# Kernel tuning notes

Hardware: AMD Instinct MI355X
Metric: run time of the kernel (lower is better)

Reference implementation:

```python
import jax, jax.numpy as jnp
import numpy as np

H = 8          # heads
D = 512        # d_model
DK = D // H    # per-head dim
FF = 2048      # feed-forward size
STACKS = 3
VOCAB = 5000
PAD = 0
LN_EPS = 1e-6


def _layer_norm(x, g, b):
    mu = jnp.mean(x, axis=-1, keepdims=True)
    var = jnp.mean(jnp.square(x - mu), axis=-1, keepdims=True)
    return (x - mu) * jax.lax.rsqrt(var + LN_EPS) * g + b


def _positional_encoding(T, d):
    pos = jnp.arange(T, dtype=jnp.float32)[:, None]                      # (T,1)
    div = jnp.exp(jnp.arange(0, d, 2, dtype=jnp.float32) * (-np.log(10000.0) / d))
    pe = jnp.zeros((T, d), dtype=jnp.float32)
    pe = pe.at[:, 0::2].set(jnp.sin(pos * div))
    pe = pe.at[:, 1::2].set(jnp.cos(pos * div))
    return pe  # (T, D)


def _mha(q_in, kv, wq, bq, wk, bk, wv, bv, wo, bo, mask):
    B, Tq, _ = q_in.shape
    Tk = kv.shape[1]
    q = (q_in @ wq + bq).reshape(B, Tq, H, DK).transpose(0, 2, 1, 3)   # (B,H,Tq,DK)
    k = (kv @ wk + bk).reshape(B, Tk, H, DK).transpose(0, 2, 1, 3)
    v = (kv @ wv + bv).reshape(B, Tk, H, DK).transpose(0, 2, 1, 3)
    score = jnp.einsum('bhqd,bhkd->bhqk', q, k) / jnp.sqrt(jnp.float32(DK))
    if mask is not None:
        score = jnp.where(mask, score, jnp.float32(-1e9))
    p = jax.nn.softmax(score, axis=-1)
    out = jnp.einsum('bhqk,bhkd->bhqd', p, v)
    out = out.transpose(0, 2, 1, 3).reshape(B, Tq, D)
    return out @ wo + bo


def setup_inputs() -> dict:
    key = jax.random.key(0)
    ks = jax.random.split(key, 24)
    s = 0.02
    inp = {
        'target': jax.random.randint(ks[0], (32, 256), 0, VOCAB),
        'memory': jax.random.normal(ks[1], (32, 1024, D), dtype=jnp.float32),
        'emb': jax.random.normal(ks[2], (VOCAB, D), dtype=jnp.float32) * s,
        'ln_g': jnp.ones((D,), jnp.float32),
        'ln_b': jnp.zeros((D,), jnp.float32),
        'ff_w1': jax.random.normal(ks[3], (D, FF), jnp.float32) * s,
        'ff_b1': jnp.zeros((FF,), jnp.float32),
        'ff_w2': jax.random.normal(ks[4], (FF, D), jnp.float32) * s,
        'ff_b2': jnp.zeros((D,), jnp.float32),
    }
    names = ['wq', 'wk', 'wv', 'wo']
    for i, n in enumerate(names):
        inp['sa_' + n] = jax.random.normal(ks[5 + i], (D, D), jnp.float32) * s
        inp['sa_b' + n[1]] = jnp.zeros((D,), jnp.float32)
        inp['ca_' + n] = jax.random.normal(ks[9 + i], (D, D), jnp.float32) * s
        inp['ca_b' + n[1]] = jnp.zeros((D,), jnp.float32)
    return inp


def reference(target, memory, emb, ln_g, ln_b, ff_w1, ff_b1, ff_w2, ff_b2,
              sa_wq, sa_bq, sa_wk, sa_bk, sa_wv, sa_bv, sa_wo, sa_bo,
              ca_wq, ca_bq, ca_wk, ca_bk, ca_wv, ca_bv, ca_wo, ca_bo):
    B, T = target.shape
    x = emb[target] * jnp.sqrt(jnp.float32(D))              # (B,T,D)
    x = x + _positional_encoding(T, D)                       # dropout = identity (eval)
    # masks: causal & pad for self-attn; cross-attn mask is all-ones -> skip
    pad = (target != PAD)[:, None, :, None]                  # (B,1,T,1)
    causal = jnp.tril(jnp.ones((T, T), dtype=bool))          # (T,T)
    tgt_mask = pad & causal                                  # (B,1,T,T)
    out = x
    for _ in range(STACKS):  # shared parameters
        n = _layer_norm(out, ln_g, ln_b)
        out = out + _mha(n, n, sa_wq, sa_bq, sa_wk, sa_bk, sa_wv, sa_bv, sa_wo, sa_bo, tgt_mask)
        n = _layer_norm(out, ln_g, ln_b)
        out = out + _mha(n, memory, ca_wq, ca_bq, ca_wk, ca_bk, ca_wv, ca_bv, ca_wo, ca_bo, None)
        n = _layer_norm(out, ln_g, ln_b)
        out = out + (jax.nn.relu(n @ ff_w1 + ff_b1) @ ff_w2 + ff_b2)
    return _layer_norm(out, ln_g, ln_b)
```

## Files before the change

kernel.cpp:

```cpp
#include <hip/hip_runtime.h>
#include <cstdint>
#include <cstddef>

typedef unsigned short u16;
typedef __bf16 bf16x8 __attribute__((ext_vector_type(8)));
typedef float f32x4 __attribute__((ext_vector_type(4)));

#define DEV static __device__ __forceinline__

#define QSCALE 0.18033688011112042f

DEV u16 f2bf(float f) { unsigned v; __builtin_memcpy(&v, &f, 4); v += 0x7fffu + ((v >> 16) & 1u); return (u16)(v >> 16); }

DEV void gll16(const void* g, void* l) {
    __builtin_amdgcn_global_load_lds(
        (__attribute__((address_space(1))) void*)g,
        (__attribute__((address_space(3))) void*)l, 16, 0, 0);
}

__global__ void embed_pe(const int* __restrict__ tgt, const float* __restrict__ emb,
                         float* __restrict__ x)
{
    const int bt = blockIdx.x;
    const int t  = bt & 255;
    const int tok = tgt[bt];
    for (int d = threadIdx.x; d < 512; d += 256) {
        float e  = emb[(size_t)tok * 512 + d] * 22.62741699796952f;
        int   d0 = d & ~1;
        float ang = (float)t * expf((float)d0 * (-9.210340371976184f / 512.f));
        float pe  = (d & 1) ? cosf(ang) : sinf(ang);
        x[(size_t)bt * 512 + d] = e + pe;
    }
}

__global__ void transpose_k(const float* __restrict__ in, u16* __restrict__ out,
                            int K, int N)
{
    int id = blockIdx.x * 256 + threadIdx.x;
    int k = id / N, n = id % N;
    out[(size_t)n * K + k] = f2bf(in[id]);
}

__global__ void memcast(const float* __restrict__ in, u16* __restrict__ out)
{
    int i = (blockIdx.x * 256 + threadIdx.x) * 4;
    float4 v = *(const float4*)(in + i);
    uint2 w;
    w.x = (unsigned)f2bf(v.x) | ((unsigned)f2bf(v.y) << 16);
    w.y = (unsigned)f2bf(v.z) | ((unsigned)f2bf(v.w) << 16);
    *(uint2*)(out + i) = w;
}

__global__ void concat_bias(const float* __restrict__ a, const float* __restrict__ b,
                            float* __restrict__ out)
{
    int i = blockIdx.x * 256 + threadIdx.x;
    if (i < 512) { out[i] = a[i]; out[512 + i] = b[i]; }
}

template<bool OUTF32>
__global__ void layernorm_k(const float* __restrict__ x, const float* __restrict__ g,
                            const float* __restrict__ b, void* __restrict__ outv)
{
    const int row  = blockIdx.x * 4 + (threadIdx.x >> 6);
    const int lane = threadIdx.x & 63;
    const float* xr = x + (size_t)row * 512;
    float4 v0 = *(const float4*)(xr + lane * 4);
    float4 v1 = *(const float4*)(xr + 256 + lane * 4);
    float s = v0.x + v0.y + v0.z + v0.w + v1.x + v1.y + v1.z + v1.w;
    float q = v0.x*v0.x + v0.y*v0.y + v0.z*v0.z + v0.w*v0.w
            + v1.x*v1.x + v1.y*v1.y + v1.z*v1.z + v1.w*v1.w;
#pragma unroll
    for (int o = 1; o < 64; o <<= 1) { s += __shfl_xor(s, o, 64); q += __shfl_xor(q, o, 64); }
    float mu  = s * (1.f / 512.f);
    float var = q * (1.f / 512.f) - mu * mu;
    float rs  = rsqrtf(fmaxf(var, 0.f) + 1e-6f);

#pragma unroll
    for (int h = 0; h < 2; h++) {
        const int d0 = h * 256 + lane * 4;
        float4 v = h ? v1 : v0;
        float4 gg = *(const float4*)(g + d0);
        float4 bb = *(const float4*)(b + d0);
        float o0 = (v.x - mu) * rs * gg.x + bb.x;
        float o1 = (v.y - mu) * rs * gg.y + bb.y;
        float o2 = (v.z - mu) * rs * gg.z + bb.z;
        float o3 = (v.w - mu) * rs * gg.w + bb.w;
        if (OUTF32) {
            *(float4*)((float*)outv + (size_t)row * 512 + d0) = make_float4(o0, o1, o2, o3);
        } else {
            uint2 w;
            w.x = (unsigned)f2bf(o0) | ((unsigned)f2bf(o1) << 16);
            w.y = (unsigned)f2bf(o2) | ((unsigned)f2bf(o3) << 16);
            *(uint2*)((u16*)outv + (size_t)row * 512 + d0) = w;
        }
    }
}

template<bool OUTF32>
__global__ void ln_sum_k(const float* __restrict__ x, const float* __restrict__ p,
                         const float* __restrict__ g, const float* __restrict__ b,
                         float* __restrict__ xout, void* __restrict__ outv)
{
    const int row  = blockIdx.x * 4 + (threadIdx.x >> 6);
    const int lane = threadIdx.x & 63;
    const size_t base = (size_t)row * 512;
    const float* xr = x + base;
    const float* pa = p + base;
    const float* pb = p + 4194304 + base;
    float4 v0, v1;
    {
        float4 a = *(const float4*)(xr + lane * 4);
        float4 c = *(const float4*)(pa + lane * 4);
        float4 d = *(const float4*)(pb + lane * 4);
        v0 = make_float4(a.x + c.x + d.x, a.y + c.y + d.y, a.z + c.z + d.z, a.w + c.w + d.w);
        a = *(const float4*)(xr + 256 + lane * 4);
        c = *(const float4*)(pa + 256 + lane * 4);
        d = *(const float4*)(pb + 256 + lane * 4);
        v1 = make_float4(a.x + c.x + d.x, a.y + c.y + d.y, a.z + c.z + d.z, a.w + c.w + d.w);
    }
    float s = v0.x + v0.y + v0.z + v0.w + v1.x + v1.y + v1.z + v1.w;
    float q = v0.x*v0.x + v0.y*v0.y + v0.z*v0.z + v0.w*v0.w
            + v1.x*v1.x + v1.y*v1.y + v1.z*v1.z + v1.w*v1.w;
#pragma unroll
    for (int o = 1; o < 64; o <<= 1) { s += __shfl_xor(s, o, 64); q += __shfl_xor(q, o, 64); }
    float mu  = s * (1.f / 512.f);
    float var = q * (1.f / 512.f) - mu * mu;
    float rs  = rsqrtf(fmaxf(var, 0.f) + 1e-6f);

#pragma unroll
    for (int h = 0; h < 2; h++) {
        const int d0 = h * 256 + lane * 4;
        float4 v = h ? v1 : v0;
        if (!OUTF32) *(float4*)(xout + base + d0) = v;
        float4 gg = *(const float4*)(g + d0);
        float4 bb = *(const float4*)(b + d0);
        float o0 = (v.x - mu) * rs * gg.x + bb.x;
        float o1 = (v.y - mu) * rs * gg.y + bb.y;
        float o2 = (v.z - mu) * rs * gg.z + bb.z;
        float o3 = (v.w - mu) * rs * gg.w + bb.w;
        if (OUTF32) {
            *(float4*)((float*)outv + base + d0) = make_float4(o0, o1, o2, o3);
        } else {
            uint2 w;
            w.x = (unsigned)f2bf(o0) | ((unsigned)f2bf(o1) << 16);
            w.y = (unsigned)f2bf(o2) | ((unsigned)f2bf(o3) << 16);
            *(uint2*)((u16*)outv + base + d0) = w;
        }
    }
}

template<int EPI, bool BROW, int BN, int QS, int SPLIT>
__launch_bounds__(256, BN == 64 ? 4 : 2)
__global__ void gemm_bt(const u16* __restrict__ A, int lda,
                        const u16* __restrict__ Bt,
                        const float* __restrict__ bias,
                        void* __restrict__ outp, int ldo, int K)
{
    constexpr int NJ = BN / 32;
    __shared__ u16 As[128 * 32];
    __shared__ u16 Bs[BN * 32];

    const int gx = gridDim.x, gy = gridDim.y;
    const int nwg = gx * gy * gridDim.z;
    int lin = blockIdx.x + gx * (blockIdx.y + gy * blockIdx.z);
    lin = (lin & 7) * (nwg >> 3) + (lin >> 3);
    const int bx = lin % gx;
    const int rem = lin / gx;
    const int by = rem % gy;
    const int bz = rem / gy;

    const int tid  = threadIdx.x;
    const int lane = tid & 63;
    const int wave = tid >> 6;
    const int quad = lane >> 4, l16 = lane & 15;
    const int l4 = lane >> 2, c8 = (lane & 3) * 8;
    const int m0 = by * 128, n0 = bx * BN;
    const int wm = (wave >> 1) * 64, wn = (wave & 1) * (BN / 2);

    const int kc = K / SPLIT;
    const int kbeg = bz * kc;

    f32x4 acc[4][NJ];
#pragma unroll
    for (int i = 0; i < 4; i++)
#pragma unroll
        for (int j = 0; j < NJ; j++) acc[i][j] = f32x4{0.f, 0.f, 0.f, 0.f};

    for (int k0 = kbeg; k0 < kbeg + kc; k0 += 32) {
        __syncthreads();
        gll16(&A[(size_t)(m0 + wave * 32 + l4)      * lda + k0 + c8], &As[(wave * 32) * 32]);
        gll16(&A[(size_t)(m0 + wave * 32 + 16 + l4) * lda + k0 + c8], &As[(wave * 32 + 16) * 32]);
        if (BN == 128) {
            gll16(&Bt[(size_t)(n0 + wave * 32 + l4)      * K + k0 + c8], &Bs[(wave * 32) * 32]);
            gll16(&Bt[(size_t)(n0 + wave * 32 + 16 + l4) * K + k0 + c8], &Bs[(wave * 32 + 16) * 32]);
        } else {
            gll16(&Bt[(size_t)(n0 + wave * 16 + l4) * K + k0 + c8], &Bs[(wave * 16) * 32]);
        }
        __syncthreads();
        bf16x8 af[4], bfr[NJ];
#pragma unroll
        for (int i = 0; i < 4; i++) af[i]  = *(const bf16x8*)&As[(wm + i * 16 + l16) * 32 + quad * 8];
#pragma unroll
        for (int j = 0; j < NJ; j++) bfr[j] = *(const bf16x8*)&Bs[(wn + j * 16 + l16) * 32 + quad * 8];
#pragma unroll
        for (int i = 0; i < 4; i++)
#pragma unroll
            for (int j = 0; j < NJ; j++)
                acc[i][j] = __builtin_amdgcn_mfma_f32_16x16x32_bf16(af[i], bfr[j], acc[i][j], 0, 0, 0);
    }

    const bool dobias = (SPLIT == 1) || (bz == 0);
#pragma unroll
    for (int i = 0; i < 4; i++)
#pragma unroll
        for (int j = 0; j < NJ; j++) {
            const int col = n0 + wn + j * 16 + l16;
            const float bc = BROW ? 0.f : (dobias ? bias[col] : 0.f);
#pragma unroll
            for (int r = 0; r < 4; r++) {
                const int row = m0 + wm + i * 16 + quad * 4 + r;
                const float bv = BROW ? (dobias ? bias[row] : 0.f) : bc;
                float v = acc[i][j][r] + bv;
                if (QS == 1) v *= QSCALE;
                if (QS == 2 && col < 512) v *= QSCALE;
                if (EPI == 1) v = fmaxf(v, 0.f);
                if (EPI == 3) {
                    ((float*)outp)[(size_t)bz * 8192 * ldo + (size_t)row * ldo + col] = v;
                } else {
                    ((u16*)outp)[(size_t)row * ldo + col] = f2bf(v);
                }
            }
        }
}

template<bool SELF>
__launch_bounds__(256, 4)
__global__ void attn(const u16* __restrict__ Qb, int qs,
                     const u16* __restrict__ Kb, int ks, int koff,
                     const u16* __restrict__ Vt, int ldv,
                     const int* __restrict__ target,
                     u16* __restrict__ Ob, int Tk)
{
    __shared__ u16 KsL[64 * 32], KsH[64 * 32];
    __shared__ u16 VsL[64 * 32], VsH[64 * 32];
    __shared__ float P32[4][16][68];
    __shared__ int needtail;
    const int tid  = threadIdx.x;
    const int lane = tid & 63;
    const int wave = tid >> 6;
    const int quad = lane >> 4, l16 = lane & 15;
    const int l4 = lane >> 2, c8 = (lane & 3) * 8;
    const int b = blockIdx.x, h = blockIdx.y, qz = blockIdx.z;
    const int qbase = qz * 64 + wave * 16;
    const int hq = h * 64;

    if (tid == 0) needtail = 0;

    const u16* qr = Qb + (size_t)(b * 256 + qbase + l16) * qs + hq;
    bf16x8 qf0 = *(const bf16x8*)(qr + quad * 8);
    bf16x8 qf1 = *(const bf16x8*)(qr + 32 + quad * 8);

    f32x4 o[4];
#pragma unroll
    for (int t = 0; t < 4; t++) o[t] = f32x4{0.f, 0.f, 0.f, 0.f};
    float ps = 0.f;
    bool rv[4];
    bool inv = false;
    if (SELF) {
#pragma unroll
        for (int r = 0; r < 4; r++) {
            rv[r] = (target[b * 256 + qbase + quad * 4 + r] != 0);
            inv |= !rv[r];
        }
    }
    const bool winv = SELF ? __any(inv) : false;
    __syncthreads();
    if (winv && lane == 0) needtail = 1;
    __syncthreads();
    const int nch = SELF ? (needtail ? (Tk >> 6) : (qz + 1)) : (Tk >> 6);

    const u16* kbase = Kb + (size_t)b * Tk * ks + koff + hq;
    const u16* vbase = Vt + (size_t)hq * ldv + (size_t)b * Tk;
    float* pw = &P32[wave][0][0];

    for (int c = 0; c < nch; c++) {
        const int k0 = c * 64;
        __syncthreads();
        gll16(kbase + (size_t)(k0 + wave * 16 + l4) * ks + c8,      &KsL[(wave * 16) * 32]);
        gll16(kbase + (size_t)(k0 + wave * 16 + l4) * ks + 32 + c8, &KsH[(wave * 16) * 32]);
        gll16(vbase + (size_t)(wave * 16 + l4) * ldv + k0 + c8,      &VsL[(wave * 16) * 32]);
        gll16(vbase + (size_t)(wave * 16 + l4) * ldv + k0 + 32 + c8, &VsH[(wave * 16) * 32]);
        __syncthreads();

        float s[4][4];
#pragma unroll
        for (int g = 0; g < 4; g++) {
            bf16x8 kf0 = *(const bf16x8*)&KsL[(g * 16 + l16) * 32 + quad * 8];
            bf16x8 kf1 = *(const bf16x8*)&KsH[(g * 16 + l16) * 32 + quad * 8];
            f32x4 sv = f32x4{0.f, 0.f, 0.f, 0.f};
            sv = __builtin_amdgcn_mfma_f32_16x16x32_bf16(qf0, kf0, sv, 0, 0, 0);
            sv = __builtin_amdgcn_mfma_f32_16x16x32_bf16(qf1, kf1, sv, 0, 0, 0);
#pragma unroll
            for (int r = 0; r < 4; r++) s[g][r] = sv[r];
        }
        if (SELF) {
            if (k0 + 64 > qbase) {
#pragma unroll
                for (int g = 0; g < 4; g++)
#pragma unroll
                    for (int r = 0; r < 4; r++)
                        if (k0 + g * 16 + l16 > qbase + quad * 4 + r) s[g][r] = -1e9f;
            }
            if (winv) {
#pragma unroll
                for (int g = 0; g < 4; g++)
#pragma unroll
                    for (int r = 0; r < 4; r++)
                        if (!rv[r]) s[g][r] = 0.f;
            }
        }
#pragma unroll
        for (int g = 0; g < 4; g++)
#pragma unroll
            for (int r = 0; r < 4; r++)
                pw[(quad * 4 + r) * 68 + g * 16 + l16] = s[g][r];
        f32x4 ra0 = *(const f32x4*)&pw[l16 * 68 + quad * 8];
        f32x4 ra1 = *(const f32x4*)&pw[l16 * 68 + quad * 8 + 4];
        f32x4 rb0 = *(const f32x4*)&pw[l16 * 68 + 32 + quad * 8];
        f32x4 rb1 = *(const f32x4*)&pw[l16 * 68 + 36 + quad * 8];
        bf16x8 pa0, pa1;
#pragma unroll
        for (int j = 0; j < 4; j++) { float p = exp2f(ra0[j]); ps += p; pa0[j]     = (__bf16)p; }
#pragma unroll
        for (int j = 0; j < 4; j++) { float p = exp2f(ra1[j]); ps += p; pa0[4 + j] = (__bf16)p; }
#pragma unroll
        for (int j = 0; j < 4; j++) { float p = exp2f(rb0[j]); ps += p; pa1[j]     = (__bf16)p; }
#pragma unroll
        for (int j = 0; j < 4; j++) { float p = exp2f(rb1[j]); ps += p; pa1[4 + j] = (__bf16)p; }
#pragma unroll
        for (int t = 0; t < 4; t++) {
            bf16x8 vf0 = *(const bf16x8*)&VsL[(t * 16 + l16) * 32 + quad * 8];
            bf16x8 vf1 = *(const bf16x8*)&VsH[(t * 16 + l16) * 32 + quad * 8];
            o[t] = __builtin_amdgcn_mfma_f32_16x16x32_bf16(pa0, vf0, o[t], 0, 0, 0);
            o[t] = __builtin_amdgcn_mfma_f32_16x16x32_bf16(pa1, vf1, o[t], 0, 0, 0);
        }
    }

    ps += __shfl_xor(ps, 16, 64);
    ps += __shfl_xor(ps, 32, 64);
#pragma unroll
    for (int r = 0; r < 4; r++) {
        const float inv_l = 1.f / __shfl(ps, quad * 4 + r, 64);
        const int tq = qbase + quad * 4 + r;
        u16* orow = Ob + (size_t)(b * 256 + tq) * 512 + hq;
#pragma unroll
        for (int t = 0; t < 4; t++) orow[t * 16 + l16] = f2bf(o[t][r] * inv_l);
    }
}

#define O_X      ((size_t)0)
#define O_N      ((size_t)16777216)
#define O_QK     ((size_t)25165824)
#define O_VTS    ((size_t)41943040)
#define O_ATT    ((size_t)50331648)
#define O_FFN    ((size_t)58720256)
#define O_KVC    ((size_t)92274688)
#define O_VTC    ((size_t)125829120)
#define O_WQKT   ((size_t)159383552)
#define O_SAVT   ((size_t)160432128)
#define O_WOT    ((size_t)160956416)
#define O_CAQT   ((size_t)161480704)
#define O_CAKT   ((size_t)162004992)
#define O_CAVT   ((size_t)162529280)
#define O_CAWOT  ((size_t)163053568)
#define O_FF1T   ((size_t)163577856)
#define O_FF2T   ((size_t)165675008)
#define O_BQK    ((size_t)167772160)

extern "C" void kernel_launch(void* const* d_in, const int* in_sizes, int n_in,
                              void* d_out, int out_size, void* d_ws, size_t ws_size,
                              hipStream_t stream)
{
    const int*   target = (const int*)d_in[0];
    const float* memory = (const float*)d_in[1];
    const float* emb    = (const float*)d_in[2];
    const float* ln_g   = (const float*)d_in[3];
    const float* ln_b   = (const float*)d_in[4];
    const float* ff_w1  = (const float*)d_in[5];
    const float* ff_b1  = (const float*)d_in[6];
    const float* ff_w2  = (const float*)d_in[7];
    const float* ff_b2  = (const float*)d_in[8];
    const float* sa_wq  = (const float*)d_in[9];
    const float* sa_bq  = (const float*)d_in[10];
    const float* ca_wq  = (const float*)d_in[11];
    const float* ca_bq  = (const float*)d_in[12];
    const float* sa_wk  = (const float*)d_in[13];
    const float* sa_bk  = (const float*)d_in[14];
    const float* ca_wk  = (const float*)d_in[15];
    const float* ca_bk  = (const float*)d_in[16];
    const float* sa_wv  = (const float*)d_in[17];
    const float* sa_bv  = (const float*)d_in[18];
    const float* ca_wv  = (const float*)d_in[19];
    const float* ca_bv  = (const float*)d_in[20];
    const float* sa_wo  = (const float*)d_in[21];
    const float* sa_bo  = (const float*)d_in[22];
    const float* ca_wo  = (const float*)d_in[23];
    const float* ca_bo  = (const float*)d_in[24];

    char* ws = (char*)d_ws;
    float* xf   = (float*)(ws + O_X);
    u16* nbuf   = (u16*)(ws + O_N);
    u16* qk     = (u16*)(ws + O_QK);
    u16* qbuf   = (u16*)(ws + O_QK);
    float* ffp  = (float*)(ws + O_QK);
    u16* vts    = (u16*)(ws + O_VTS);
    u16* att    = (u16*)(ws + O_ATT);
    u16* ffn    = (u16*)(ws + O_FFN);
    u16* membf  = (u16*)(ws + O_FFN);
    float* wop  = (float*)(ws + O_FFN);
    u16* kvc    = (u16*)(ws + O_KVC);
    u16* vtc    = (u16*)(ws + O_VTC);
    u16* wqkt   = (u16*)(ws + O_WQKT);
    u16* savt   = (u16*)(ws + O_SAVT);
    u16* wot    = (u16*)(ws + O_WOT);
    u16* caqt   = (u16*)(ws + O_CAQT);
    u16* cakt   = (u16*)(ws + O_CAKT);
    u16* cavt   = (u16*)(ws + O_CAVT);
    u16* cawot  = (u16*)(ws + O_CAWOT);
    u16* ff1t   = (u16*)(ws + O_FF1T);
    u16* ff2t   = (u16*)(ws + O_FF2T);
    float* bqk  = (float*)(ws + O_BQK);

    transpose_k<<<1024, 256, 0, stream>>>(sa_wq, wqkt,             512, 512);
    transpose_k<<<1024, 256, 0, stream>>>(sa_wk, wqkt + 512 * 512, 512, 512);
    transpose_k<<<1024, 256, 0, stream>>>(sa_wv, savt,  512, 512);
    transpose_k<<<1024, 256, 0, stream>>>(sa_wo, wot,   512, 512);
    transpose_k<<<1024, 256, 0, stream>>>(ca_wq, caqt,  512, 512);
    transpose_k<<<1024, 256, 0, stream>>>(ca_wk, cakt,  512, 512);
    transpose_k<<<1024, 256, 0, stream>>>(ca_wv, cavt,  512, 512);
    transpose_k<<<1024, 256, 0, stream>>>(ca_wo, cawot, 512, 512);
    transpose_k<<<4096, 256, 0, stream>>>(ff_w1, ff1t,  512, 2048);
    transpose_k<<<4096, 256, 0, stream>>>(ff_w2, ff2t, 2048, 512);
    concat_bias<<<2, 256, 0, stream>>>(sa_bq, sa_bk, bqk);

    embed_pe<<<8192, 256, 0, stream>>>(target, emb, xf);

    memcast<<<16384, 256, 0, stream>>>(memory, membf);
    gemm_bt<0, false, 64, 0, 1><<<dim3(8, 256), 256, 0, stream>>>(membf, 512, cakt, ca_bk, kvc, 512, 512);
    gemm_bt<0, true,  64, 0, 1><<<dim3(512, 4), 256, 0, stream>>>(cavt, 512, membf, ca_bv, vtc, 32768, 512);

    for (int s = 0; s < 3; s++) {
        if (s == 0)
            layernorm_k<false><<<2048, 256, 0, stream>>>(xf, ln_g, ln_b, nbuf);
        else
            ln_sum_k<false><<<2048, 256, 0, stream>>>(xf, ffp, ln_g, ln_b, xf, nbuf);
        gemm_bt<0, false, 64, 2, 1><<<dim3(16, 64), 256, 0, stream>>>(nbuf, 512, wqkt, bqk, qk, 1024, 512);
        gemm_bt<0, true,  64, 0, 1><<<dim3(128, 4), 256, 0, stream>>>(savt, 512, nbuf, sa_bv, vts, 8192, 512);
        attn<true><<<dim3(32, 8, 4), 256, 0, stream>>>(qk, 1024, qk, 1024, 512, vts, 8192, target, att, 256);
        gemm_bt<3, false, 64, 0, 2><<<dim3(8, 64, 2), 256, 0, stream>>>(att, 512, wot, sa_bo, wop, 512, 512);
        ln_sum_k<false><<<2048, 256, 0, stream>>>(xf, wop, ln_g, ln_b, xf, nbuf);
        gemm_bt<0, false, 64, 1, 1><<<dim3(8, 64), 256, 0, stream>>>(nbuf, 512, caqt, ca_bq, qbuf, 512, 512);
        attn<false><<<dim3(32, 8, 4), 256, 0, stream>>>(qbuf, 512, kvc, 512, 0, vtc, 32768, nullptr, att, 1024);
        gemm_bt<3, false, 64, 0, 2><<<dim3(8, 64, 2), 256, 0, stream>>>(att, 512, cawot, ca_bo, wop, 512, 512);
        ln_sum_k<false><<<2048, 256, 0, stream>>>(xf, wop, ln_g, ln_b, xf, nbuf);
        gemm_bt<1, false, 64, 0, 1><<<dim3(32, 64), 256, 0, stream>>>(nbuf, 512, ff1t, ff_b1, ffn, 2048, 512);
        gemm_bt<3, false, 64, 0, 2><<<dim3(8, 64, 2), 256, 0, stream>>>(ffn, 2048, ff2t, ff_b2, ffp, 512, 2048);
    }

    ln_sum_k<true><<<2048, 256, 0, stream>>>(xf, ffp, ln_g, ln_b, xf, d_out);
}
```

Baseline: 926.1 us.

## Process two query tiles per attention block with double-buffered K/V loads

The attention kernel now handles two 64-query tiles per block, so each K/V chunk staged in LDS is reused across twice as many query rows. K/V chunks are double-buffered, with the next chunk's async global-to-LDS load issued before computing the current one, leaving one barrier per iteration. Grid z is halved and launch bounds are relaxed to 2 blocks, which lowers parallelism and coarsens causal chunk skipping in exchange for less load traffic and better overlap.

```diff
diff --git a/kernel.cpp b/kernel.cpp
--- a/kernel.cpp
+++ b/kernel.cpp
@@ -234,16 +234,15 @@
         }
 }
 
-template<bool SELF>
-__launch_bounds__(256, 4)
+template<bool SELF, int QT>
+__launch_bounds__(256, 2)
 __global__ void attn(const u16* __restrict__ Qb, int qs,
                      const u16* __restrict__ Kb, int ks, int koff,
                      const u16* __restrict__ Vt, int ldv,
                      const int* __restrict__ target,
                      u16* __restrict__ Ob, int Tk)
 {
-    __shared__ u16 KsL[64 * 32], KsH[64 * 32];
-    __shared__ u16 VsL[64 * 32], VsH[64 * 32];
+    __shared__ u16 KV[2][4][64 * 32];
     __shared__ float P32[4][16][68];
     __shared__ int needtail;
     const int tid  = threadIdx.x;
@@ -252,110 +251,153 @@
     const int quad = lane >> 4, l16 = lane & 15;
     const int l4 = lane >> 2, c8 = (lane & 3) * 8;
     const int b = blockIdx.x, h = blockIdx.y, qz = blockIdx.z;
-    const int qbase = qz * 64 + wave * 16;
     const int hq = h * 64;
 
     if (tid == 0) needtail = 0;
 
-    const u16* qr = Qb + (size_t)(b * 256 + qbase + l16) * qs + hq;
-    bf16x8 qf0 = *(const bf16x8*)(qr + quad * 8);
-    bf16x8 qf1 = *(const bf16x8*)(qr + 32 + quad * 8);
-
-    f32x4 o[4];
-#pragma unroll
-    for (int t = 0; t < 4; t++) o[t] = f32x4{0.f, 0.f, 0.f, 0.f};
-    float ps = 0.f;
-    bool rv[4];
-    bool inv = false;
+    int qbase[QT];
+    bf16x8 qf0[QT], qf1[QT];
+#pragma unroll
+    for (int i = 0; i < QT; i++) {
+        qbase[i] = qz * (64 * QT) + (wave + 4 * i) * 16;
+        const u16* qr = Qb + (size_t)(b * 256 + qbase[i] + l16) * qs + hq;
+        qf0[i] = *(const bf16x8*)(qr + quad * 8);
+        qf1[i] = *(const bf16x8*)(qr + 32 + quad * 8);
+    }
+
+    f32x4 o[QT][4];
+#pragma unroll
+    for (int i = 0; i < QT; i++)
+#pragma unroll
+        for (int t = 0; t < 4; t++) o[i][t] = f32x4{0.f, 0.f, 0.f, 0.f};
+    float ps[QT];
+#pragma unroll
+    for (int i = 0; i < QT; i++) ps[i] = 0.f;
+
+    bool rv[QT][4];
+    bool tpad[QT];
+    bool anyinv = false;
+#pragma unroll
+    for (int i = 0; i < QT; i++) tpad[i] = false;
     if (SELF) {
 #pragma unroll
-        for (int r = 0; r < 4; r++) {
-            rv[r] = (target[b * 256 + qbase + quad * 4 + r] != 0);
-            inv |= !rv[r];
-        }
-    }
-    const bool winv = SELF ? __any(inv) : false;
+        for (int i = 0; i < QT; i++) {
+            bool inv = false;
+#pragma unroll
+            for (int r = 0; r < 4; r++) {
+                rv[i][r] = (target[b * 256 + qbase[i] + quad * 4 + r] != 0);
+                inv |= !rv[i][r];
+            }
+            tpad[i] = __any(inv);
+            anyinv |= tpad[i];
+        }
+    }
     __syncthreads();
-    if (winv && lane == 0) needtail = 1;
-    __syncthreads();
-    const int nch = SELF ? (needtail ? (Tk >> 6) : (qz + 1)) : (Tk >> 6);
+    if (anyinv && lane == 0) needtail = 1;
 
     const u16* kbase = Kb + (size_t)b * Tk * ks + koff + hq;
     const u16* vbase = Vt + (size_t)hq * ldv + (size_t)b * Tk;
     float* pw = &P32[wave][0][0];
 
+    {
+        gll16(kbase + (size_t)(wave * 16 + l4) * ks + c8,      &KV[0][0][(wave * 16) * 32]);
+        gll16(kbase + (size_t)(wave * 16 + l4) * ks + 32 + c8, &KV[0][1][(wave * 16) * 32]);
+        gll16(vbase + (size_t)(wave * 16 + l4) * ldv + c8,      &KV[0][2][(wave * 16) * 32]);
+        gll16(vbase + (size_t)(wave * 16 + l4) * ldv + 32 + c8, &KV[0][3][(wave * 16) * 32]);
+    }
+    __syncthreads();
+    const int nch = SELF ? (needtail ? (Tk >> 6) : QT * (qz + 1)) : (Tk >> 6);
+
     for (int c = 0; c < nch; c++) {
+        const int cur = c & 1;
         const int k0 = c * 64;
+        if (c + 1 < nch) {
+            const int kn = (c + 1) * 64;
+            gll16(kbase + (size_t)(kn + wave * 16 + l4) * ks + c8,      &KV[cur ^ 1][0][(wave * 16) * 32]);
+            gll16(kbase + (size_t)(kn + wave * 16 + l4) * ks + 32 + c8, &KV[cur ^ 1][1][(wave * 16) * 32]);
+            gll16(vbase + (size_t)(wave * 16 + l4) * ldv + kn + c8,      &KV[cur ^ 1][2][(wave * 16) * 32]);
+            gll16(vbase + (size_t)(wave * 16 + l4) * ldv + kn + 32 + c8, &KV[cur ^ 1][3][(wave * 16) * 32]);
+        }
+        const u16* KsLc = KV[cur][0];
+        const u16* KsHc = KV[cur][1];
+        const u16* VsLc = KV[cur][2];
+        const u16* VsHc = KV[cur][3];
+
+#pragma unroll
+        for (int i = 0; i < QT; i++) {
+            if (SELF && !((qbase[i] + 16 > k0) || tpad[i])) continue;
+
+            float s[4][4];
+#pragma unroll
+            for (int g = 0; g < 4; g++) {
+                bf16x8 kf0 = *(const bf16x8*)&KsLc[(g * 16 + l16) * 32 + quad * 8];
+                bf16x8 kf1 = *(const bf16x8*)&KsHc[(g * 16 + l16) * 32 + quad * 8];
+                f32x4 sv = f32x4{0.f, 0.f, 0.f, 0.f};
+                sv = __builtin_amdgcn_mfma_f32_16x16x32_bf16(qf0[i], kf0, sv, 0, 0, 0);
+                sv = __builtin_amdgcn_mfma_f32_16x16x32_bf16(qf1[i], kf1, sv, 0, 0, 0);
+#pragma unroll
+                for (int r = 0; r < 4; r++) s[g][r] = sv[r];
+            }
+            if (SELF) {
+                if (k0 + 64 > qbase[i]) {
+#pragma unroll
+                    for (int g = 0; g < 4; g++)
+#pragma unroll
+                        for (int r = 0; r < 4; r++)
+                            if (k0 + g * 16 + l16 > qbase[i] + quad * 4 + r) s[g][r] = -1e9f;
+                }
+                if (tpad[i]) {
+#pragma unroll
+                    for (int g = 0; g < 4; g++)
+#pragma unroll
+                        for (int r = 0; r < 4; r++)
+                            if (!rv[i][r]) s[g][r] = 0.f;
+                }
+            }
+#pragma unroll
+            for (int g = 0; g < 4; g++)
+#pragma unroll
+                for (int r = 0; r < 4; r++)
+                    pw[(quad * 4 + r) * 68 + g * 16 + l16] = s[g][r];
+            f32x4 ra0 = *(const f32x4*)&pw[l16 * 68 + quad * 8];
+            f32x4 ra1 = *(const f32x4*)&pw[l16 * 68 + quad * 8 + 4];
+            f32x4 rb0 = *(const f32x4*)&pw[l16 * 68 + 32 + quad * 8];
+            f32x4 rb1 = *(const f32x4*)&pw[l16 * 68 + 36 + quad * 8];
+            bf16x8 pa0, pa1;
+            float pls = 0.f;
+#pragma unroll
+            for (int j = 0; j < 4; j++) { float p = exp2f(ra0[j]); pls += p; pa0[j]     = (__bf16)p; }
+#pragma unroll
+            for (int j = 0; j < 4; j++) { float p = exp2f(ra1[j]); pls += p; pa0[4 + j] = (__bf16)p; }
+#pragma unroll
+            for (int j = 0; j < 4; j++) { float p = exp2f(rb0[j]); pls += p; pa1[j]     = (__bf16)p; }
+#pragma unroll
+            for (int j = 0; j < 4; j++) { float p = exp2f(rb1[j]); pls += p; pa1[4 + j] = (__bf16)p; }
+            ps[i] += pls;
+#pragma unroll
+            for (int t = 0; t < 4; t++) {
+                bf16x8 vf0 = *(const bf16x8*)&VsLc[(t * 16 + l16) * 32 + quad * 8];
+                bf16x8 vf1 = *(const bf16x8*)&VsHc[(t * 16 + l16) * 32 + quad * 8];
+                o[i][t] = __builtin_amdgcn_mfma_f32_16x16x32_bf16(pa0, vf0, o[i][t], 0, 0, 0);
+                o[i][t] = __builtin_amdgcn_mfma_f32_16x16x32_bf16(pa1, vf1, o[i][t], 0, 0, 0);
+            }
+        }
         __syncthreads();
-        gll16(kbase + (size_t)(k0 + wave * 16 + l4) * ks + c8,      &KsL[(wave * 16) * 32]);
-        gll16(kbase + (size_t)(k0 + wave * 16 + l4) * ks + 32 + c8, &KsH[(wave * 16) * 32]);
-        gll16(vbase + (size_t)(wave * 16 + l4) * ldv + k0 + c8,      &VsL[(wave * 16) * 32]);
-        gll16(vbase + (size_t)(wave * 16 + l4) * ldv + k0 + 32 + c8, &VsH[(wave * 16) * 32]);
-        __syncthreads();
-
-        float s[4][4];
-#pragma unroll
-        for (int g = 0; g < 4; g++) {
-            bf16x8 kf0 = *(const bf16x8*)&KsL[(g * 16 + l16) * 32 + quad * 8];
-            bf16x8 kf1 = *(const bf16x8*)&KsH[(g * 16 + l16) * 32 + quad * 8];
-            f32x4 sv = f32x4{0.f, 0.f, 0.f, 0.f};
-            sv = __builtin_amdgcn_mfma_f32_16x16x32_bf16(qf0, kf0, sv, 0, 0, 0);
-            sv = __builtin_amdgcn_mfma_f32_16x16x32_bf16(qf1, kf1, sv, 0, 0, 0);
-#pragma unroll
-            for (int r = 0; r < 4; r++) s[g][r] = sv[r];
-        }
-        if (SELF) {
-            if (k0 + 64 > qbase) {
-#pragma unroll
-                for (int g = 0; g < 4; g++)
-#pragma unroll
-                    for (int r = 0; r < 4; r++)
-                        if (k0 + g * 16 + l16 > qbase + quad * 4 + r) s[g][r] = -1e9f;
-            }
-            if (winv) {
-#pragma unroll
-                for (int g = 0; g < 4; g++)
-#pragma unroll
-                    for (int r = 0; r < 4; r++)
-                        if (!rv[r]) s[g][r] = 0.f;
-            }
-        }
-#pragma unroll
-        for (int g = 0; g < 4; g++)
-#pragma unroll
-            for (int r = 0; r < 4; r++)
-                pw[(quad * 4 + r) * 68 + g * 16 + l16] = s[g][r];
-        f32x4 ra0 = *(const f32x4*)&pw[l16 * 68 + quad * 8];
-        f32x4 ra1 = *(const f32x4*)&pw[l16 * 68 + quad * 8 + 4];
-        f32x4 rb0 = *(const f32x4*)&pw[l16 * 68 + 32 + quad * 8];
-        f32x4 rb1 = *(const f32x4*)&pw[l16 * 68 + 36 + quad * 8];
-        bf16x8 pa0, pa1;
-#pragma unroll
-        for (int j = 0; j < 4; j++) { float p = exp2f(ra0[j]); ps += p; pa0[j]     = (__bf16)p; }
-#pragma unroll
-        for (int j = 0; j < 4; j++) { float p = exp2f(ra1[j]); ps += p; pa0[4 + j] = (__bf16)p; }
-#pragma unroll
-        for (int j = 0; j < 4; j++) { float p = exp2f(rb0[j]); ps += p; pa1[j]     = (__bf16)p; }
-#pragma unroll
-        for (int j = 0; j < 4; j++) { float p = exp2f(rb1[j]); ps += p; pa1[4 + j] = (__bf16)p; }
-#pragma unroll
-        for (int t = 0; t < 4; t++) {
-            bf16x8 vf0 = *(const bf16x8*)&VsL[(t * 16 + l16) * 32 + quad * 8];
-            bf16x8 vf1 = *(const bf16x8*)&VsH[(t * 16 + l16) * 32 + quad * 8];
-            o[t] = __builtin_amdgcn_mfma_f32_16x16x32_bf16(pa0, vf0, o[t], 0, 0, 0);
-            o[t] = __builtin_amdgcn_mfma_f32_16x16x32_bf16(pa1, vf1, o[t], 0, 0, 0);
-        }
-    }
-
-    ps += __shfl_xor(ps, 16, 64);
-    ps += __shfl_xor(ps, 32, 64);
-#pragma unroll
-    for (int r = 0; r < 4; r++) {
-        const float inv_l = 1.f / __shfl(ps, quad * 4 + r, 64);
-        const int tq = qbase + quad * 4 + r;
-        u16* orow = Ob + (size_t)(b * 256 + tq) * 512 + hq;
-#pragma unroll
-        for (int t = 0; t < 4; t++) orow[t * 16 + l16] = f2bf(o[t][r] * inv_l);
+    }
+
+#pragma unroll
+    for (int i = 0; i < QT; i++) {
+        float p = ps[i];
+        p += __shfl_xor(p, 16, 64);
+        p += __shfl_xor(p, 32, 64);
+#pragma unroll
+        for (int r = 0; r < 4; r++) {
+            const float inv_l = 1.f / __shfl(p, quad * 4 + r, 64);
+            const int tq = qbase[i] + quad * 4 + r;
+            u16* orow = Ob + (size_t)(b * 256 + tq) * 512 + hq;
+#pragma unroll
+            for (int t = 0; t < 4; t++) orow[t * 16 + l16] = f2bf(o[i][t][r] * inv_l);
+        }
     }
 }
 
@@ -457,11 +499,11 @@
             ln_sum_k<false><<<2048, 256, 0, stream>>>(xf, ffp, ln_g, ln_b, xf, nbuf);
         gemm_bt<0, false, 64, 2, 1><<<dim3(16, 64), 256, 0, stream>>>(nbuf, 512, wqkt, bqk, qk, 1024, 512);
         gemm_bt<0, true,  64, 0, 1><<<dim3(128, 4), 256, 0, stream>>>(savt, 512, nbuf, sa_bv, vts, 8192, 512);
-        attn<true><<<dim3(32, 8, 4), 256, 0, stream>>>(qk, 1024, qk, 1024, 512, vts, 8192, target, att, 256);
+        attn<true, 2><<<dim3(32, 8, 2), 256, 0, stream>>>(qk, 1024, qk, 1024, 512, vts, 8192, target, att, 256);
         gemm_bt<3, false, 64, 0, 2><<<dim3(8, 64, 2), 256, 0, stream>>>(att, 512, wot, sa_bo, wop, 512, 512);
         ln_sum_k<false><<<2048, 256, 0, stream>>>(xf, wop, ln_g, ln_b, xf, nbuf);
         gemm_bt<0, false, 64, 1, 1><<<dim3(8, 64), 256, 0, stream>>>(nbuf, 512, caqt, ca_bq, qbuf, 512, 512);
-        attn<false><<<dim3(32, 8, 4), 256, 0, stream>>>(qbuf, 512, kvc, 512, 0, vtc, 32768, nullptr, att, 1024);
+        attn<false, 2><<<dim3(32, 8, 2), 256, 0, stream>>>(qbuf, 512, kvc, 512, 0, vtc, 32768, nullptr, att, 1024);
         gemm_bt<3, false, 64, 0, 2><<<dim3(8, 64, 2), 256, 0, stream>>>(att, 512, cawot, ca_bo, wop, 512, 512);
         ln_sum_k<false><<<2048, 256, 0, stream>>>(xf, wop, ln_g, ln_b, xf, nbuf);
         gemm_bt<1, false, 64, 0, 1><<<dim3(32, 64), 256, 0, stream>>>(nbuf, 512, ff1t, ff_b1, ffn, 2048, 512);
```

Result: no change. 931.2 us (+0.5%).

## Double-buffer K/V tiles in attention with 8-wave blocks and swizzled LDS

Applied to the files above, without the earlier changes.

Rewrites the attention kernel to use 512-thread blocks covering 128 query rows, so each staged K/V chunk is shared by twice as many waves. K/V loads now go into a double buffer and are prefetched one chunk ahead, with one barrier per iteration instead of two. The score tile is written to LDS directly as bf16 after exp2, dropping the fp32 round-trip, and an XOR swizzle is applied to LDS column offsets to reduce bank conflicts. Causal waves skip fully masked chunks, but the grid now has half as many blocks, which lowers parallelism, and the bigger blocks may affect occupancy.

```diff
diff --git a/kernel.cpp b/kernel.cpp
--- a/kernel.cpp
+++ b/kernel.cpp
@@ -235,25 +235,24 @@
 }
 
 template<bool SELF>
-__launch_bounds__(256, 4)
+__launch_bounds__(512, 4)
 __global__ void attn(const u16* __restrict__ Qb, int qs,
                      const u16* __restrict__ Kb, int ks, int koff,
                      const u16* __restrict__ Vt, int ldv,
                      const int* __restrict__ target,
                      u16* __restrict__ Ob, int Tk)
 {
-    __shared__ u16 KsL[64 * 32], KsH[64 * 32];
-    __shared__ u16 VsL[64 * 32], VsH[64 * 32];
-    __shared__ float P32[4][16][68];
+    __shared__ u16 KV[2][4][64 * 32];
+    __shared__ __align__(16) __bf16 P16[8][16 * 72];
     __shared__ int needtail;
     const int tid  = threadIdx.x;
     const int lane = tid & 63;
     const int wave = tid >> 6;
     const int quad = lane >> 4, l16 = lane & 15;
-    const int l4 = lane >> 2, c8 = (lane & 3) * 8;
     const int b = blockIdx.x, h = blockIdx.y, qz = blockIdx.z;
-    const int qbase = qz * 64 + wave * 16;
+    const int qbase = qz * 128 + wave * 16;
     const int hq = h * 64;
+    const int kcol = ((quad ^ ((l16 >> 1) & 3)) * 8);
 
     if (tid == 0) needtail = 0;
 
@@ -264,94 +263,114 @@
     f32x4 o[4];
 #pragma unroll
     for (int t = 0; t < 4; t++) o[t] = f32x4{0.f, 0.f, 0.f, 0.f};
-    float ps = 0.f;
+    float pr[4] = {0.f, 0.f, 0.f, 0.f};
+
     bool rv[4];
-    bool inv = false;
+    bool tpad = false;
     if (SELF) {
+        bool inv = false;
 #pragma unroll
         for (int r = 0; r < 4; r++) {
             rv[r] = (target[b * 256 + qbase + quad * 4 + r] != 0);
             inv |= !rv[r];
         }
-    }
-    const bool winv = SELF ? __any(inv) : false;
-    __syncthreads();
-    if (winv && lane == 0) needtail = 1;
-    __syncthreads();
-    const int nch = SELF ? (needtail ? (Tk >> 6) : (qz + 1)) : (Tk >> 6);
+        tpad = __any(inv);
+    }
 
     const u16* kbase = Kb + (size_t)b * Tk * ks + koff + hq;
     const u16* vbase = Vt + (size_t)hq * ldv + (size_t)b * Tk;
-    float* pw = &P32[wave][0][0];
+    __bf16* pw = P16[wave];
+
+    const int srow0 = ((wave * 2) & 3) * 16 + (lane >> 2);
+    const int srow1 = ((wave * 2 + 1) & 3) * 16 + (lane >> 2);
+    const int sc0 = (((lane & 3) ^ ((srow0 >> 1) & 3)) * 8);
+    const int sc1 = (((lane & 3) ^ ((srow1 >> 1) & 3)) * 8);
+    const int arr0 = (wave * 2) >> 2, arr1 = (wave * 2 + 1) >> 2;
+    u16* ldst0;  u16* ldst1;
+
+#define STAGE_KV(buf, k0)                                                        \
+    {                                                                            \
+        const u16* src0; const u16* src1;                                        \
+        if (arr0 == 0)      src0 = kbase + (size_t)((k0) + srow0) * ks + sc0;    \
+        else if (arr0 == 1) src0 = kbase + (size_t)((k0) + srow0) * ks + 32 + sc0;\
+        else if (arr0 == 2) src0 = vbase + (size_t)srow0 * ldv + (k0) + sc0;     \
+        else                src0 = vbase + (size_t)srow0 * ldv + (k0) + 32 + sc0;\
+        if (arr1 == 0)      src1 = kbase + (size_t)((k0) + srow1) * ks + sc1;    \
+        else if (arr1 == 1) src1 = kbase + (size_t)((k0) + srow1) * ks + 32 + sc1;\
+        else if (arr1 == 2) src1 = vbase + (size_t)srow1 * ldv + (k0) + sc1;     \
+        else                src1 = vbase + (size_t)srow1 * ldv + (k0) + 32 + sc1;\
+        ldst0 = &KV[buf][arr0][(((wave * 2) & 3) * 16) * 32];                    \
+        ldst1 = &KV[buf][arr1][(((wave * 2 + 1) & 3) * 16) * 32];                \
+        gll16(src0, ldst0);                                                      \
+        gll16(src1, ldst1);                                                      \
+    }
+
+    STAGE_KV(0, 0)
+    __syncthreads();
+    if (SELF && tpad && lane == 0) needtail = 1;
+    __syncthreads();
+    const int nch = SELF ? (needtail ? (Tk >> 6) : 2 * (qz + 1)) : (Tk >> 6);
 
     for (int c = 0; c < nch; c++) {
+        const int cur = c & 1;
         const int k0 = c * 64;
+        if (c + 1 < nch) STAGE_KV(cur ^ 1, (c + 1) * 64)
+
+        const u16* KsLc = KV[cur][0];
+        const u16* KsHc = KV[cur][1];
+        const u16* VsLc = KV[cur][2];
+        const u16* VsHc = KV[cur][3];
+
+        const bool active = !SELF || (qbase + 16 > k0) || tpad;
+        if (active) {
+#pragma unroll
+            for (int g = 0; g < 4; g++) {
+                bf16x8 kf0 = *(const bf16x8*)&KsLc[(g * 16 + l16) * 32 + kcol];
+                bf16x8 kf1 = *(const bf16x8*)&KsHc[(g * 16 + l16) * 32 + kcol];
+                f32x4 sv = f32x4{0.f, 0.f, 0.f, 0.f};
+                sv = __builtin_amdgcn_mfma_f32_16x16x32_bf16(qf0, kf0, sv, 0, 0, 0);
+                sv = __builtin_amdgcn_mfma_f32_16x16x32_bf16(qf1, kf1, sv, 0, 0, 0);
+                if (SELF) {
+                    if (k0 + 64 > qbase) {
+#pragma unroll
+                        for (int r = 0; r < 4; r++)
+                            if (k0 + g * 16 + l16 > qbase + quad * 4 + r) sv[r] = -1e9f;
+                    }
+                    if (tpad) {
+#pragma unroll
+                        for (int r = 0; r < 4; r++)
+                            if (!rv[r]) sv[r] = 0.f;
+                    }
+                }
+#pragma unroll
+                for (int r = 0; r < 4; r++) {
+                    float p = exp2f(sv[r]);
+                    pr[r] += p;
+                    pw[(quad * 4 + r) * 72 + g * 16 + l16] = (__bf16)p;
+                }
+            }
+            bf16x8 pa0 = *(const bf16x8*)&pw[l16 * 72 + quad * 8];
+            bf16x8 pa1 = *(const bf16x8*)&pw[l16 * 72 + 32 + quad * 8];
+#pragma unroll
+            for (int t = 0; t < 4; t++) {
+                bf16x8 vf0 = *(const bf16x8*)&VsLc[(t * 16 + l16) * 32 + kcol];
+                bf16x8 vf1 = *(const bf16x8*)&VsHc[(t * 16 + l16) * 32 + kcol];
+                o[t] = __builtin_amdgcn_mfma_f32_16x16x32_bf16(pa0, vf0, o[t], 0, 0, 0);
+                o[t] = __builtin_amdgcn_mfma_f32_16x16x32_bf16(pa1, vf1, o[t], 0, 0, 0);
+            }
+        }
         __syncthreads();
-        gll16(kbase + (size_t)(k0 + wave * 16 + l4) * ks + c8,      &KsL[(wave * 16) * 32]);
-        gll16(kbase + (size_t)(k0 + wave * 16 + l4) * ks + 32 + c8, &KsH[(wave * 16) * 32]);
-        gll16(vbase + (size_t)(wave * 16 + l4) * ldv + k0 + c8,      &VsL[(wave * 16) * 32]);
-        gll16(vbase + (size_t)(wave * 16 + l4) * ldv + k0 + 32 + c8, &VsH[(wave * 16) * 32]);
-        __syncthreads();
-
-        float s[4][4];
-#pragma unroll
-        for (int g = 0; g < 4; g++) {
-            bf16x8 kf0 = *(const bf16x8*)&KsL[(g * 16 + l16) * 32 + quad * 8];
-            bf16x8 kf1 = *(const bf16x8*)&KsH[(g * 16 + l16) * 32 + quad * 8];
-            f32x4 sv = f32x4{0.f, 0.f, 0.f, 0.f};
-            sv = __builtin_amdgcn_mfma_f32_16x16x32_bf16(qf0, kf0, sv, 0, 0, 0);
-            sv = __builtin_amdgcn_mfma_f32_16x16x32_bf16(qf1, kf1, sv, 0, 0, 0);
-#pragma unroll
-            for (int r = 0; r < 4; r++) s[g][r] = sv[r];
-        }
-        if (SELF) {
-            if (k0 + 64 > qbase) {
-#pragma unroll
-                for (int g = 0; g < 4; g++)
-#pragma unroll
-                    for (int r = 0; r < 4; r++)
-                        if (k0 + g * 16 + l16 > qbase + quad * 4 + r) s[g][r] = -1e9f;
-            }
-            if (winv) {
-#pragma unroll
-                for (int g = 0; g < 4; g++)
-#pragma unroll
-                    for (int r = 0; r < 4; r++)
-                        if (!rv[r]) s[g][r] = 0.f;
-            }
-        }
-#pragma unroll
-        for (int g = 0; g < 4; g++)
-#pragma unroll
-            for (int r = 0; r < 4; r++)
-                pw[(quad * 4 + r) * 68 + g * 16 + l16] = s[g][r];
-        f32x4 ra0 = *(const f32x4*)&pw[l16 * 68 + quad * 8];
-        f32x4 ra1 = *(const f32x4*)&pw[l16 * 68 + quad * 8 + 4];
-        f32x4 rb0 = *(const f32x4*)&pw[l16 * 68 + 32 + quad * 8];
-        f32x4 rb1 = *(const f32x4*)&pw[l16 * 68 + 36 + quad * 8];
-        bf16x8 pa0, pa1;
-#pragma unroll
-        for (int j = 0; j < 4; j++) { float p = exp2f(ra0[j]); ps += p; pa0[j]     = (__bf16)p; }
-#pragma unroll
-        for (int j = 0; j < 4; j++) { float p = exp2f(ra1[j]); ps += p; pa0[4 + j] = (__bf16)p; }
-#pragma unroll
-        for (int j = 0; j < 4; j++) { float p = exp2f(rb0[j]); ps += p; pa1[j]     = (__bf16)p; }
-#pragma unroll
-        for (int j = 0; j < 4; j++) { float p = exp2f(rb1[j]); ps += p; pa1[4 + j] = (__bf16)p; }
-#pragma unroll
-        for (int t = 0; t < 4; t++) {
-            bf16x8 vf0 = *(const bf16x8*)&VsL[(t * 16 + l16) * 32 + quad * 8];
-            bf16x8 vf1 = *(const bf16x8*)&VsH[(t * 16 + l16) * 32 + quad * 8];
-            o[t] = __builtin_amdgcn_mfma_f32_16x16x32_bf16(pa0, vf0, o[t], 0, 0, 0);
-            o[t] = __builtin_amdgcn_mfma_f32_16x16x32_bf16(pa1, vf1, o[t], 0, 0, 0);
-        }
-    }
-
-    ps += __shfl_xor(ps, 16, 64);
-    ps += __shfl_xor(ps, 32, 64);
+    }
+#undef STAGE_KV
+
 #pragma unroll
     for (int r = 0; r < 4; r++) {
-        const float inv_l = 1.f / __shfl(ps, quad * 4 + r, 64);
+#pragma unroll
+        for (int off = 1; off < 16; off <<= 1) pr[r] += __shfl_xor(pr[r], off, 64);
+    }
+#pragma unroll
+    for (int r = 0; r < 4; r++) {
+        const float inv_l = 1.f / pr[r];
         const int tq = qbase + quad * 4 + r;
         u16* orow = Ob + (size_t)(b * 256 + tq) * 512 + hq;
 #pragma unroll
@@ -457,11 +476,11 @@
             ln_sum_k<false><<<2048, 256, 0, stream>>>(xf, ffp, ln_g, ln_b, xf, nbuf);
         gemm_bt<0, false, 64, 2, 1><<<dim3(16, 64), 256, 0, stream>>>(nbuf, 512, wqkt, bqk, qk, 1024, 512);
         gemm_bt<0, true,  64, 0, 1><<<dim3(128, 4), 256, 0, stream>>>(savt, 512, nbuf, sa_bv, vts, 8192, 512);
-        attn<true><<<dim3(32, 8, 4), 256, 0, stream>>>(qk, 1024, qk, 1024, 512, vts, 8192, target, att, 256);
+        attn<true><<<dim3(32, 8, 2), 512, 0, stream>>>(qk, 1024, qk, 1024, 512, vts, 8192, target, att, 256);
         gemm_bt<3, false, 64, 0, 2><<<dim3(8, 64, 2), 256, 0, stream>>>(att, 512, wot, sa_bo, wop, 512, 512);
         ln_sum_k<false><<<2048, 256, 0, stream>>>(xf, wop, ln_g, ln_b, xf, nbuf);
         gemm_bt<0, false, 64, 1, 1><<<dim3(8, 64), 256, 0, stream>>>(nbuf, 512, caqt, ca_bq, qbuf, 512, 512);
-        attn<false><<<dim3(32, 8, 4), 256, 0, stream>>>(qbuf, 512, kvc, 512, 0, vtc, 32768, nullptr, att, 1024);
+        attn<false><<<dim3(32, 8, 2), 512, 0, stream>>>(qbuf, 512, kvc, 512, 0, vtc, 32768, nullptr, att, 1024);
         gemm_bt<3, false, 64, 0, 2><<<dim3(8, 64, 2), 256, 0, stream>>>(att, 512, cawot, ca_bo, wop, 512, 512);
         ln_sum_k<false><<<2048, 256, 0, stream>>>(xf, wop, ln_g, ln_b, xf, nbuf);
         gemm_bt<1, false, 64, 0, 1><<<dim3(32, 64), 256, 0, stream>>>(nbuf, 512, ff1t, ff_b1, ffn, 2048, 512);
```

After: 918.7 us. About the same (-0.8%).
